# Kernel optimization log

Hardware: AMD Instinct MI355X
Metric: run time of the kernel (lower is better)

## Reference

```python
import jax, jax.numpy as jnp
import numpy as np

N_NODES = 100000
N_EDGES = 1600000
D_FEAT = 128
HIDDEN = 128
N_CLASSES = 10
NUM_GRAPHS = 64


def setup_inputs() -> dict:
    key = jax.random.key(0)
    ks = jax.random.split(key, 12)
    x = jax.random.normal(ks[0], (N_NODES, D_FEAT), dtype=jnp.float32)
    edge_index = jax.random.randint(ks[1], (2, N_EDGES), 0, N_NODES, dtype=jnp.int32)
    batch = jnp.sort(jax.random.randint(ks[2], (N_NODES,), 0, NUM_GRAPHS, dtype=jnp.int32))
    s = 1.0 / np.sqrt(HIDDEN)
    def lin(k, out_d, in_d):
        return jax.random.uniform(k, (out_d, in_d), jnp.float32, -s, s)
    return {
        "x": x,
        "edge_index": edge_index,
        "batch": batch,
        "W1l": lin(ks[3], HIDDEN, D_FEAT), "b1": jnp.zeros((HIDDEN,), jnp.float32),
        "W1r": lin(ks[4], HIDDEN, D_FEAT),
        "W2l": lin(ks[5], HIDDEN, HIDDEN), "b2": jnp.zeros((HIDDEN,), jnp.float32),
        "W2r": lin(ks[6], HIDDEN, HIDDEN),
        "W3l": lin(ks[7], HIDDEN, HIDDEN), "b3": jnp.zeros((HIDDEN,), jnp.float32),
        "W3r": lin(ks[8], HIDDEN, HIDDEN),
        "Wout": lin(ks[9], N_CLASSES, HIDDEN), "bout": jnp.zeros((N_CLASSES,), jnp.float32),
    }


def reference(x, edge_index, batch, W1l, b1, W1r, W2l, b2, W2r, W3l, b3, W3r, Wout, bout):
    src, dst = edge_index[0], edge_index[1]
    n = x.shape[0]

    def sage(h, Wl, b, Wr):
        # sum-aggregate neighbor features: scatter-add x[src] into dst rows
        agg = jax.ops.segment_sum(h[src], dst, num_segments=n)  # [N, d]
        return agg @ Wl.T + b + h @ Wr.T

    h = jax.nn.relu(sage(x, W1l, b1, W1r))
    h = jax.nn.relu(sage(h, W2l, b2, W2r))
    h = sage(h, W3l, b3, W3r)
    pooled = jax.ops.segment_sum(h, batch, num_segments=NUM_GRAPHS)  # [G, hidden]
    # dropout is identity in eval mode
    return pooled @ Wout.T + bout
```

## Files before the change

kernel.cpp:

```cpp
#include <hip/hip_runtime.h>
#include <hip/hip_bf16.h>

#define N_NODES  100000
#define N_EDGES  1600000
#define D_FEAT   128
#define HIDDEN   128
#define N_CLASSES 10
#define NUM_GRAPHS 64

#define NBUCK 250
#define NPB   400
#define CHUNK 12500

typedef __bf16 bf16x8 __attribute__((ext_vector_type(8)));
typedef float  f32x4  __attribute__((ext_vector_type(4)));

static __device__ __forceinline__ unsigned short f2bf(float f) {
    __bf16 b = (__bf16)f;
    return __builtin_bit_cast(unsigned short, b);
}

__global__ void conv_w6_kernel(const float* __restrict__ W0, const float* __restrict__ W1,
                               const float* __restrict__ W2, const float* __restrict__ W3,
                               const float* __restrict__ W4, const float* __restrict__ W5,
                               __bf16* __restrict__ out) {
    const float* Ws[6] = {W0, W1, W2, W3, W4, W5};
    int m = blockIdx.x >> 6;
    int i = (blockIdx.x & 63) * 256 + threadIdx.x;
    out[m * (HIDDEN * D_FEAT) + i] = (__bf16)Ws[m][i];
}

__global__ __launch_bounds__(256) void bucket_hist_kernel(const int* __restrict__ ei,
                                                          int* __restrict__ bh) {
    __shared__ int h[NBUCK];
    int t = threadIdx.x;
    for (int i = t; i < NBUCK; i += 256) h[i] = 0;
    __syncthreads();
    int e0 = blockIdx.x * CHUNK;
    for (int e = e0 + t; e < e0 + CHUNK; e += 256) {
        int d = ei[N_EDGES + e];
        atomicAdd(&h[d / NPB], 1);
    }
    __syncthreads();
    for (int i = t; i < NBUCK; i += 256) atomicAdd(&bh[i], h[i]);
}

__global__ __launch_bounds__(256) void bucket_scan_kernel(const int* __restrict__ bh,
                                                          int* __restrict__ bbase,
                                                          int* __restrict__ bcur) {
    __shared__ int tmp[256];
    int t = threadIdx.x;
    int v = (t < NBUCK) ? bh[t] : 0;
    tmp[t] = v;
    __syncthreads();
    for (int off = 1; off < 256; off <<= 1) {
        int x = (t >= off) ? tmp[t - off] : 0;
        __syncthreads();
        tmp[t] += x;
        __syncthreads();
    }
    if (t < NBUCK) { int e = tmp[t] - v; bbase[t] = e; bcur[t] = e; }
    if (t == NBUCK - 1) bbase[NBUCK] = tmp[t];
}

__global__ __launch_bounds__(256) void bucket_scatter_kernel(const int* __restrict__ ei,
                                                             int* __restrict__ bcur,
                                                             int2* __restrict__ bkt) {
    __shared__ int h[NBUCK];
    __shared__ int lbase[NBUCK];
    int t = threadIdx.x;
    for (int i = t; i < NBUCK; i += 256) h[i] = 0;
    __syncthreads();
    int e0 = blockIdx.x * CHUNK;
    for (int e = e0 + t; e < e0 + CHUNK; e += 256) {
        int d = ei[N_EDGES + e];
        atomicAdd(&h[d / NPB], 1);
    }
    __syncthreads();
    for (int i = t; i < NBUCK; i += 256) {
        lbase[i] = atomicAdd(&bcur[i], h[i]);
        h[i] = 0;
    }
    __syncthreads();
    for (int e = e0 + t; e < e0 + CHUNK; e += 256) {
        int s = ei[e];
        int d = ei[N_EDGES + e];
        int bb = d / NPB;
        int pos = lbase[bb] + atomicAdd(&h[bb], 1);
        bkt[pos] = make_int2(s, d);
    }
}

__global__ __launch_bounds__(256) void bucket_csr_kernel(const int2* __restrict__ bkt,
                                                         const int* __restrict__ bbase,
                                                         int* __restrict__ rp,
                                                         int* __restrict__ csr_src) {
    const int b = blockIdx.x;
    const int n0 = b * NPB;
    const int ebase = bbase[b], eend = bbase[b + 1];
    __shared__ int cnt[NPB];
    __shared__ int part[128];
    __shared__ int excl[NPB];
    int t = threadIdx.x;
    for (int i = t; i < NPB; i += 256) cnt[i] = 0;
    __syncthreads();
    for (int e = ebase + t; e < eend; e += 256) {
        int2 p = bkt[e];
        atomicAdd(&cnt[p.y - n0], 1);
    }
    __syncthreads();
    int gs = 0;
    if (t < 100) { gs = cnt[4 * t] + cnt[4 * t + 1] + cnt[4 * t + 2] + cnt[4 * t + 3]; part[t] = gs; }
    else if (t < 128) part[t] = 0;
    __syncthreads();
    for (int off = 1; off < 128; off <<= 1) {
        int x = 0;
        if (t < 128 && t >= off) x = part[t - off];
        __syncthreads();
        if (t < 128) part[t] += x;
        __syncthreads();
    }
    if (t < 100) part[t] -= gs;
    __syncthreads();
    for (int i = t; i < NPB; i += 256) {
        int g = i >> 2;
        int e0 = part[g];
        for (int j = g * 4; j < i; j++) e0 += cnt[j];
        excl[i] = e0;
    }
    __syncthreads();
    for (int i = t; i < NPB; i += 256) {
        rp[n0 + i] = ebase + excl[i];
        cnt[i] = excl[i];
    }
    if (b == NBUCK - 1 && t == 0) rp[N_NODES] = N_EDGES;
    __syncthreads();
    for (int e = ebase + t; e < eend; e += 256) {
        int2 p = bkt[e];
        int pos = ebase + atomicAdd(&cnt[p.y - n0], 1);
        csr_src[pos] = p.x;
    }
}

template<bool ABF16>
__global__ __launch_bounds__(256) void dual_gemm_kernel(
    const void* __restrict__ hv,
    const __bf16* __restrict__ Wl, const __bf16* __restrict__ Wr,
    const float* __restrict__ bias,
    __bf16* __restrict__ out_l, __bf16* __restrict__ out_r, int M)
{
    const int wave = threadIdx.x >> 6;
    const int lane = threadIdx.x & 63;
    const int kq = lane >> 4;
    const int ln = lane & 15;
    const int node_base = blockIdx.x * 64;
    const int f_base = wave * 32;

    bf16x8 wfrag[2][2][4];
    #pragma unroll
    for (int t = 0; t < 2; t++) {
        int wrow = f_base + t * 16 + ln;
        #pragma unroll
        for (int kc = 0; kc < 4; kc++) {
            int k0 = kc * 32 + kq * 8;
            wfrag[0][t][kc] = *(const bf16x8*)(Wl + wrow * 128 + k0);
            wfrag[1][t][kc] = *(const bf16x8*)(Wr + wrow * 128 + k0);
        }
    }
    float4 bias4[2];
    bias4[0] = *(const float4*)(bias + f_base + kq * 4);
    bias4[1] = *(const float4*)(bias + f_base + 16 + kq * 4);

    #pragma unroll
    for (int tau = 0; tau < 4; tau++) {
        int node = node_base + tau * 16 + ln;
        int nodec = node < M ? node : (M - 1);

        bf16x8 hfrag[4];
        if constexpr (ABF16) {
            const __bf16* hrow = ((const __bf16*)hv) + (size_t)nodec * 128;
            #pragma unroll
            for (int kc = 0; kc < 4; kc++)
                hfrag[kc] = *(const bf16x8*)(hrow + kc * 32 + kq * 8);
        } else {
            const float* hrow = ((const float*)hv) + (size_t)nodec * 128;
            #pragma unroll
            for (int kc = 0; kc < 4; kc++) {
                int k0 = kc * 32 + kq * 8;
                float4 v0 = *(const float4*)(hrow + k0);
                float4 v1 = *(const float4*)(hrow + k0 + 4);
                bf16x8 a;
                a[0] = (__bf16)v0.x; a[1] = (__bf16)v0.y; a[2] = (__bf16)v0.z; a[3] = (__bf16)v0.w;
                a[4] = (__bf16)v1.x; a[5] = (__bf16)v1.y; a[6] = (__bf16)v1.z; a[7] = (__bf16)v1.w;
                hfrag[kc] = a;
            }
        }

        f32x4 accl[2] = {(f32x4)(0.f), (f32x4)(0.f)};
        f32x4 accr[2] = {(f32x4)(0.f), (f32x4)(0.f)};
        #pragma unroll
        for (int kc = 0; kc < 4; kc++) {
            #pragma unroll
            for (int t = 0; t < 2; t++) {
                accl[t] = __builtin_amdgcn_mfma_f32_16x16x32_bf16(wfrag[0][t][kc], hfrag[kc], accl[t], 0, 0, 0);
                accr[t] = __builtin_amdgcn_mfma_f32_16x16x32_bf16(wfrag[1][t][kc], hfrag[kc], accr[t], 0, 0, 0);
            }
        }

        if (node < M) {
            size_t rowoff = (size_t)node * 128;
            #pragma unroll
            for (int t = 0; t < 2; t++) {
                int fc = f_base + t * 16 + kq * 4;
                ushort4 ol;
                ol.x = f2bf(accl[t][0]); ol.y = f2bf(accl[t][1]);
                ol.z = f2bf(accl[t][2]); ol.w = f2bf(accl[t][3]);
                *(ushort4*)(out_l + rowoff + fc) = ol;
                ushort4 orr;
                orr.x = f2bf(accr[t][0] + bias4[t].x);
                orr.y = f2bf(accr[t][1] + bias4[t].y);
                orr.z = f2bf(accr[t][2] + bias4[t].z);
                orr.w = f2bf(accr[t][3] + bias4[t].w);
                *(ushort4*)(out_r + rowoff + fc) = orr;
            }
        }
    }
}

template<bool RELU>
__global__ __launch_bounds__(256) void gather_kernel(
    const __bf16* __restrict__ hl, const int* __restrict__ rp,
    const int* __restrict__ csr_src, const __bf16* __restrict__ base,
    __bf16* __restrict__ outp, int N)
{
    int nid = blockIdx.x * 16 + (threadIdx.x >> 4);
    if (nid >= N) return;
    int f8 = threadIdx.x & 15;
    int start = rp[nid], end = rp[nid + 1];

    bf16x8 b8 = ((const bf16x8*)base)[(size_t)nid * 16 + f8];
    float a[8];
    #pragma unroll
    for (int i = 0; i < 8; i++) a[i] = (float)b8[i];

    int j = start;
    for (; j + 1 < end; j += 2) {
        int s0 = csr_src[j];
        int s1 = csr_src[j + 1];
        bf16x8 u0 = ((const bf16x8*)hl)[(size_t)s0 * 16 + f8];
        bf16x8 u1 = ((const bf16x8*)hl)[(size_t)s1 * 16 + f8];
        #pragma unroll
        for (int i = 0; i < 8; i++) a[i] += (float)u0[i] + (float)u1[i];
    }
    if (j < end) {
        int s0 = csr_src[j];
        bf16x8 u0 = ((const bf16x8*)hl)[(size_t)s0 * 16 + f8];
        #pragma unroll
        for (int i = 0; i < 8; i++) a[i] += (float)u0[i];
    }
    bf16x8 o;
    #pragma unroll
    for (int i = 0; i < 8; i++) {
        float v = RELU ? fmaxf(a[i], 0.f) : a[i];
        o[i] = (__bf16)v;
    }
    ((bf16x8*)outp)[(size_t)nid * 16 + f8] = o;
}

__global__ __launch_bounds__(256) void pool_kernel(
    const __bf16* __restrict__ h, const int* __restrict__ batch,
    float* __restrict__ pooled, int N)
{
    int idx = blockIdx.x * 256 + threadIdx.x;
    int f = idx & 127;
    int chunk = idx >> 7;
    int n0 = chunk * 32;
    if (n0 >= N) return;
    int n1 = n0 + 32; if (n1 > N) n1 = N;
    int curb = batch[n0];
    float acc = 0.f;
    for (int n = n0; n < n1; n++) {
        int b = batch[n];
        if (b != curb) {
            unsafeAtomicAdd(&pooled[(size_t)curb * 128 + f], acc);
            acc = 0.f; curb = b;
        }
        acc += (float)h[(size_t)n * 128 + f];
    }
    unsafeAtomicAdd(&pooled[(size_t)curb * 128 + f], acc);
}

__global__ void final_gemm_kernel(
    const float* __restrict__ pooled, const float* __restrict__ Wout,
    const float* __restrict__ bout, float* __restrict__ out)
{
    int idx = blockIdx.x * 64 + threadIdx.x;
    if (idx < NUM_GRAPHS * N_CLASSES) {
        int g = idx / N_CLASSES;
        int c = idx % N_CLASSES;
        float acc = bout[c];
        for (int k = 0; k < HIDDEN; k++)
            acc += pooled[g * HIDDEN + k] * Wout[c * HIDDEN + k];
        out[idx] = acc;
    }
}

extern "C" void kernel_launch(void* const* d_in, const int* in_sizes, int n_in,
                              void* d_out, int out_size, void* d_ws, size_t ws_size,
                              hipStream_t stream) {
    const float* x     = (const float*)d_in[0];
    const int*   ei    = (const int*)d_in[1];
    const int*   batch = (const int*)d_in[2];
    const float* W1l = (const float*)d_in[3];
    const float* b1  = (const float*)d_in[4];
    const float* W1r = (const float*)d_in[5];
    const float* W2l = (const float*)d_in[6];
    const float* b2  = (const float*)d_in[7];
    const float* W2r = (const float*)d_in[8];
    const float* W3l = (const float*)d_in[9];
    const float* b3  = (const float*)d_in[10];
    const float* W3r = (const float*)d_in[11];
    const float* Wout = (const float*)d_in[12];
    const float* bout = (const float*)d_in[13];
    float* out = (float*)d_out;

    char* ws = (char*)d_ws;
    size_t off = 0;
    __bf16* bufL  = (__bf16*)(ws + off); off += (size_t)N_NODES * 128 * sizeof(__bf16);
    __bf16* bufR  = (__bf16*)(ws + off); off += (size_t)N_NODES * 128 * sizeof(__bf16);
    __bf16* bufH  = (__bf16*)(ws + off); off += (size_t)N_NODES * 128 * sizeof(__bf16);
    float* pooled = (float*)(ws + off);  off += (size_t)NUM_GRAPHS * HIDDEN * sizeof(float);
    __bf16* wbf   = (__bf16*)(ws + off); off += 6 * (size_t)HIDDEN * D_FEAT * sizeof(__bf16);
    int* rp       = (int*)(ws + off);    off += ((size_t)N_NODES + 16) * sizeof(int);
    int* csr_src  = (int*)(ws + off);    off += (size_t)N_EDGES * sizeof(int);
    int2* bkt     = (int2*)(ws + off);   off += (size_t)N_EDGES * sizeof(int2);
    int* bh       = (int*)(ws + off);    off += (NBUCK + 8) * sizeof(int);
    int* bbase    = (int*)(ws + off);    off += (NBUCK + 8) * sizeof(int);
    int* bcur     = (int*)(ws + off);    off += (NBUCK + 8) * sizeof(int);

    const int WSZ = HIDDEN * D_FEAT;

    conv_w6_kernel<<<6 * 64, 256, 0, stream>>>(W1l, W1r, W2l, W2r, W3l, W3r, wbf);

    hipMemsetAsync(bh, 0, NBUCK * sizeof(int), stream);
    bucket_hist_kernel<<<128, 256, 0, stream>>>(ei, bh);
    bucket_scan_kernel<<<1, 256, 0, stream>>>(bh, bbase, bcur);
    bucket_scatter_kernel<<<128, 256, 0, stream>>>(ei, bcur, bkt);
    bucket_csr_kernel<<<NBUCK, 256, 0, stream>>>(bkt, bbase, rp, csr_src);

    const int gemm_grid = (N_NODES + 63) / 64;
    const int gath_grid = (N_NODES + 15) / 16;

    dual_gemm_kernel<false><<<gemm_grid, 256, 0, stream>>>(x, wbf + 0 * WSZ, wbf + 1 * WSZ, b1, bufL, bufR, N_NODES);
    gather_kernel<true><<<gath_grid, 256, 0, stream>>>(bufL, rp, csr_src, bufR, bufH, N_NODES);

    dual_gemm_kernel<true><<<gemm_grid, 256, 0, stream>>>(bufH, wbf + 2 * WSZ, wbf + 3 * WSZ, b2, bufL, bufR, N_NODES);
    gather_kernel<true><<<gath_grid, 256, 0, stream>>>(bufL, rp, csr_src, bufR, bufH, N_NODES);

    dual_gemm_kernel<true><<<gemm_grid, 256, 0, stream>>>(bufH, wbf + 4 * WSZ, wbf + 5 * WSZ, b3, bufL, bufR, N_NODES);
    gather_kernel<false><<<gath_grid, 256, 0, stream>>>(bufL, rp, csr_src, bufR, bufH, N_NODES);

    hipMemsetAsync(pooled, 0, (size_t)NUM_GRAPHS * HIDDEN * sizeof(float), stream);
    const int pool_grid = ((N_NODES + 31) / 32 * 128 + 255) / 256;
    pool_kernel<<<pool_grid, 256, 0, stream>>>(bufH, batch, pooled, N_NODES);
    final_gemm_kernel<<<10, 64, 0, stream>>>(pooled, Wout, bout, out);
}
```

Measured before the change: 507.6 us.

## Stage GEMM input tiles in LDS via async loads, pre-convert x, unroll gather

The dual GEMM now processes 128-node tiles that are copied into LDS with global_load_lds using an XOR swizzle, instead of each wave reading rows from global memory directly. The input x is converted to bf16 once by a separate kernel so all layers share one bf16 GEMM path, and bufH is padded so the last tile can read past the end without bounds checks. The gather loop is unrolled by four to keep more independent loads in flight. The cost is an extra conversion pass over x, more LDS per block (lower occupancy), and reads of uninitialised padding rows whose results are never stored.

```diff
diff --git a/kernel.cpp b/kernel.cpp
--- a/kernel.cpp
+++ b/kernel.cpp
@@ -11,6 +11,8 @@
 #define NBUCK 250
 #define NPB   400
 #define CHUNK 12500
+#define GT    128
+#define NPAD  100096
 
 typedef __bf16 bf16x8 __attribute__((ext_vector_type(8)));
 typedef float  f32x4  __attribute__((ext_vector_type(4)));
@@ -18,6 +20,12 @@
 static __device__ __forceinline__ unsigned short f2bf(float f) {
     __bf16 b = (__bf16)f;
     return __builtin_bit_cast(unsigned short, b);
+}
+
+static __device__ __forceinline__ void async_copy16(void* lds, const void* g) {
+    __builtin_amdgcn_global_load_lds(
+        (const __attribute__((address_space(1))) void*)g,
+        (__attribute__((address_space(3))) void*)lds, 16, 0, 0);
 }
 
 __global__ void conv_w6_kernel(const float* __restrict__ W0, const float* __restrict__ W1,
@@ -28,6 +36,17 @@
     int m = blockIdx.x >> 6;
     int i = (blockIdx.x & 63) * 256 + threadIdx.x;
     out[m * (HIDDEN * D_FEAT) + i] = (__bf16)Ws[m][i];
+}
+
+__global__ __launch_bounds__(256) void xconv_kernel(const float* __restrict__ x,
+                                                    __bf16* __restrict__ out) {
+    int i = blockIdx.x * 256 + threadIdx.x;
+    float4 v0 = ((const float4*)x)[i * 2];
+    float4 v1 = ((const float4*)x)[i * 2 + 1];
+    bf16x8 o;
+    o[0] = (__bf16)v0.x; o[1] = (__bf16)v0.y; o[2] = (__bf16)v0.z; o[3] = (__bf16)v0.w;
+    o[4] = (__bf16)v1.x; o[5] = (__bf16)v1.y; o[6] = (__bf16)v1.z; o[7] = (__bf16)v1.w;
+    ((bf16x8*)out)[i] = o;
 }
 
 __global__ __launch_bounds__(256) void bucket_hist_kernel(const int* __restrict__ ei,
@@ -142,19 +161,32 @@
     }
 }
 
-template<bool ABF16>
 __global__ __launch_bounds__(256) void dual_gemm_kernel(
-    const void* __restrict__ hv,
+    const __bf16* __restrict__ h,
     const __bf16* __restrict__ Wl, const __bf16* __restrict__ Wr,
     const float* __restrict__ bias,
     __bf16* __restrict__ out_l, __bf16* __restrict__ out_r, int M)
 {
-    const int wave = threadIdx.x >> 6;
-    const int lane = threadIdx.x & 63;
+    __shared__ __bf16 tile_lds[GT * 128];
+
+    const int tid  = threadIdx.x;
+    const int wave = tid >> 6;
+    const int lane = tid & 63;
     const int kq = lane >> 4;
     const int ln = lane & 15;
-    const int node_base = blockIdx.x * 64;
+    const int node_base = blockIdx.x * GT;
     const int f_base = wave * 32;
+
+    {
+        const __bf16* hsrc = h + (size_t)node_base * 128;
+        #pragma unroll
+        for (int i = 0; i < 8; i++) {
+            int u = i * 256 + tid;
+            int row = u >> 4;
+            int sc = (u & 15) ^ (row & 15);
+            async_copy16(&tile_lds[u * 8], hsrc + row * 128 + sc * 8);
+        }
+    }
 
     bf16x8 wfrag[2][2][4];
     #pragma unroll
@@ -171,29 +203,16 @@
     bias4[0] = *(const float4*)(bias + f_base + kq * 4);
     bias4[1] = *(const float4*)(bias + f_base + 16 + kq * 4);
 
-    #pragma unroll
-    for (int tau = 0; tau < 4; tau++) {
-        int node = node_base + tau * 16 + ln;
-        int nodec = node < M ? node : (M - 1);
-
+    __syncthreads();
+
+    #pragma unroll 2
+    for (int tau = 0; tau < GT / 16; tau++) {
+        int r = tau * 16 + ln;
         bf16x8 hfrag[4];
-        if constexpr (ABF16) {
-            const __bf16* hrow = ((const __bf16*)hv) + (size_t)nodec * 128;
-            #pragma unroll
-            for (int kc = 0; kc < 4; kc++)
-                hfrag[kc] = *(const bf16x8*)(hrow + kc * 32 + kq * 8);
-        } else {
-            const float* hrow = ((const float*)hv) + (size_t)nodec * 128;
-            #pragma unroll
-            for (int kc = 0; kc < 4; kc++) {
-                int k0 = kc * 32 + kq * 8;
-                float4 v0 = *(const float4*)(hrow + k0);
-                float4 v1 = *(const float4*)(hrow + k0 + 4);
-                bf16x8 a;
-                a[0] = (__bf16)v0.x; a[1] = (__bf16)v0.y; a[2] = (__bf16)v0.z; a[3] = (__bf16)v0.w;
-                a[4] = (__bf16)v1.x; a[5] = (__bf16)v1.y; a[6] = (__bf16)v1.z; a[7] = (__bf16)v1.w;
-                hfrag[kc] = a;
-            }
+        #pragma unroll
+        for (int kc = 0; kc < 4; kc++) {
+            int c = (4 * kc + kq) ^ ln;
+            hfrag[kc] = *(const bf16x8*)&tile_lds[r * 128 + c * 8];
         }
 
         f32x4 accl[2] = {(f32x4)(0.f), (f32x4)(0.f)};
@@ -207,6 +226,7 @@
             }
         }
 
+        int node = node_base + tau * 16 + ln;
         if (node < M) {
             size_t rowoff = (size_t)node * 128;
             #pragma unroll
@@ -244,15 +264,20 @@
     for (int i = 0; i < 8; i++) a[i] = (float)b8[i];
 
     int j = start;
-    for (; j + 1 < end; j += 2) {
+    for (; j + 3 < end; j += 4) {
         int s0 = csr_src[j];
         int s1 = csr_src[j + 1];
+        int s2 = csr_src[j + 2];
+        int s3 = csr_src[j + 3];
         bf16x8 u0 = ((const bf16x8*)hl)[(size_t)s0 * 16 + f8];
         bf16x8 u1 = ((const bf16x8*)hl)[(size_t)s1 * 16 + f8];
-        #pragma unroll
-        for (int i = 0; i < 8; i++) a[i] += (float)u0[i] + (float)u1[i];
-    }
-    if (j < end) {
+        bf16x8 u2 = ((const bf16x8*)hl)[(size_t)s2 * 16 + f8];
+        bf16x8 u3 = ((const bf16x8*)hl)[(size_t)s3 * 16 + f8];
+        #pragma unroll
+        for (int i = 0; i < 8; i++)
+            a[i] += ((float)u0[i] + (float)u1[i]) + ((float)u2[i] + (float)u3[i]);
+    }
+    for (; j < end; j++) {
         int s0 = csr_src[j];
         bf16x8 u0 = ((const bf16x8*)hl)[(size_t)s0 * 16 + f8];
         #pragma unroll
@@ -328,7 +353,7 @@
     size_t off = 0;
     __bf16* bufL  = (__bf16*)(ws + off); off += (size_t)N_NODES * 128 * sizeof(__bf16);
     __bf16* bufR  = (__bf16*)(ws + off); off += (size_t)N_NODES * 128 * sizeof(__bf16);
-    __bf16* bufH  = (__bf16*)(ws + off); off += (size_t)N_NODES * 128 * sizeof(__bf16);
+    __bf16* bufH  = (__bf16*)(ws + off); off += (size_t)NPAD * 128 * sizeof(__bf16);
     float* pooled = (float*)(ws + off);  off += (size_t)NUM_GRAPHS * HIDDEN * sizeof(float);
     __bf16* wbf   = (__bf16*)(ws + off); off += 6 * (size_t)HIDDEN * D_FEAT * sizeof(__bf16);
     int* rp       = (int*)(ws + off);    off += ((size_t)N_NODES + 16) * sizeof(int);
@@ -341,6 +366,7 @@
     const int WSZ = HIDDEN * D_FEAT;
 
     conv_w6_kernel<<<6 * 64, 256, 0, stream>>>(W1l, W1r, W2l, W2r, W3l, W3r, wbf);
+    xconv_kernel<<<N_NODES * 128 / (256 * 8), 256, 0, stream>>>(x, bufH);
 
     hipMemsetAsync(bh, 0, NBUCK * sizeof(int), stream);
     bucket_hist_kernel<<<128, 256, 0, stream>>>(ei, bh);
@@ -348,16 +374,16 @@
     bucket_scatter_kernel<<<128, 256, 0, stream>>>(ei, bcur, bkt);
     bucket_csr_kernel<<<NBUCK, 256, 0, stream>>>(bkt, bbase, rp, csr_src);
 
-    const int gemm_grid = (N_NODES + 63) / 64;
+    const int gemm_grid = NPAD / GT;
     const int gath_grid = (N_NODES + 15) / 16;
 
-    dual_gemm_kernel<false><<<gemm_grid, 256, 0, stream>>>(x, wbf + 0 * WSZ, wbf + 1 * WSZ, b1, bufL, bufR, N_NODES);
+    dual_gemm_kernel<<<gemm_grid, 256, 0, stream>>>(bufH, wbf + 0 * WSZ, wbf + 1 * WSZ, b1, bufL, bufR, N_NODES);
     gather_kernel<true><<<gath_grid, 256, 0, stream>>>(bufL, rp, csr_src, bufR, bufH, N_NODES);
 
-    dual_gemm_kernel<true><<<gemm_grid, 256, 0, stream>>>(bufH, wbf + 2 * WSZ, wbf + 3 * WSZ, b2, bufL, bufR, N_NODES);
+    dual_gemm_kernel<<<gemm_grid, 256, 0, stream>>>(bufH, wbf + 2 * WSZ, wbf + 3 * WSZ, b2, bufL, bufR, N_NODES);
     gather_kernel<true><<<gath_grid, 256, 0, stream>>>(bufL, rp, csr_src, bufR, bufH, N_NODES);
 
-    dual_gemm_kernel<true><<<gemm_grid, 256, 0, stream>>>(bufH, wbf + 4 * WSZ, wbf + 5 * WSZ, b3, bufL, bufR, N_NODES);
+    dual_gemm_kernel<<<gemm_grid, 256, 0, stream>>>(bufH, wbf + 4 * WSZ, wbf + 5 * WSZ, b3, bufL, bufR, N_NODES);
     gather_kernel<false><<<gath_grid, 256, 0, stream>>>(bufL, rp, csr_src, bufR, bufH, N_NODES);
 
     hipMemsetAsync(pooled, 0, (size_t)NUM_GRAPHS * HIDDEN * sizeof(float), stream);
```

After: 471.9 us. 7.0% less time.
